# Kernel tuning notes

Measured on AMD Instinct MI355X. Metric: run time of the kernel, lower is better.

Reference implementation:

```python
import jax, jax.numpy as jnp
import numpy as np

B, T, D, K, CAND = 1024, 256, 128, 4, 500
NEG = float(-2**32 + 1)
EPS = 1e-3  # keras LayerNormalization default epsilon

def ln(x, g, b):
    mu = jnp.mean(x, axis=-1, keepdims=True)
    var = jnp.mean(jnp.square(x - mu), axis=-1, keepdims=True)
    return (x - mu) * jax.lax.rsqrt(var + EPS) * g + b

def setup_inputs() -> dict:
    key = jax.random.key(0)
    ks = jax.random.split(key, 12)
    s = 0.05
    inp = {
        'item_his_eb': jax.random.normal(ks[0], (B, T, D), jnp.float32),
        'mask': jax.random.randint(ks[1], (B, T), 0, 2, jnp.int32),
        'W1': jax.random.normal(ks[2], (D, D), jnp.float32) * s,
        'W2': jax.random.normal(ks[3], (D,), jnp.float32) * s,
        'W3': jax.random.normal(ks[4], (D, D), jnp.float32) * s,
        'W4': jax.random.normal(ks[5], (D,), jnp.float32) * s,
        'W_k1': jax.random.normal(ks[6], (K, D, D), jnp.float32) * s,
        'W_k2': jax.random.normal(ks[7], (K, D), jnp.float32) * s,
        'C': jax.random.normal(ks[8], (CAND, D), jnp.float32) * s,
        'pos_emb': jax.random.normal(ks[9], (1, T, D), jnp.float32) * s,
        'g1': jnp.ones((D,), jnp.float32), 'b1': jnp.zeros((D,), jnp.float32),
        'g2': jnp.ones((D,), jnp.float32), 'b2': jnp.zeros((D,), jnp.float32),
        'g3': jnp.ones((D,), jnp.float32), 'b3': jnp.zeros((D,), jnp.float32),
        'g4': jnp.ones((D,), jnp.float32), 'b4': jnp.zeros((D,), jnp.float32),
    }
    return inp

def reference(item_his_eb, mask, W1, W2, W3, W4, W_k1, W_k2, C, pos_emb,
              g1, b1, g2, b2, g3, b3, g4, b4):
    num_interest = W_k1.shape[0]
    m0 = (mask == 0)  # [B,T] padding positions
    x = item_his_eb + pos_emb  # [B,T,D]

    # Concept activation
    hidden = jnp.tanh(jnp.einsum('bte,ea->bta', x, W1))
    att = jnp.einsum('bte,e->bt', hidden, W2)
    a = jax.nn.softmax(jnp.where(m0, NEG, att), axis=-1)
    z_u = jnp.einsum('bte,bt->be', x, a)
    s_u = jnp.einsum('be,ce->bc', z_u, C)  # [B,CAND]
    s_u_k, idx = jax.lax.top_k(s_u, num_interest)  # sorted descending
    c_u = C[idx] * jax.nn.sigmoid(s_u_k)[..., None]  # [B,K,D]

    # Interest embedding generation
    h1 = jnp.einsum('bte,ea->bta', x, W3)
    h1 = jnp.einsum('bte,bke->btk', ln(h1, g1, b1), ln(c_u, g2, b2))
    h1 = jnp.where(m0[:, :, None], NEG, h1)
    P_kt = jnp.transpose(jax.nn.softmax(h1, axis=-1), (0, 2, 1))  # [B,K,T]
    h2 = jnp.tanh(jnp.einsum('bte,kea->bkta', x, W_k1))
    h2 = jnp.einsum('bkte,ke->bkt', h2, W_k2)
    h2 = jnp.where(m0[:, None, :], NEG, h2)
    P_tk = jax.nn.softmax(h2, axis=-1)  # softmax over t
    P = P_kt * P_tk
    interest_emb = ln(jnp.einsum('bte,bkt->bke', x, P), g3, b3)  # [B,K,D]

    # Interest aggregation
    P_u = jnp.transpose(P_kt, (0, 2, 1))  # [B,T,K]
    X_hat = jnp.einsum('btk,bke->bte', P_u, c_u)
    h3 = jnp.tanh(jnp.einsum('bte,ea->bta', X_hat, W3))
    h3 = jnp.einsum('bte,e->bt', h3, W4)
    h3 = jax.nn.softmax(jnp.where(m0, NEG, h3), axis=-1)
    c_apt = ln(jnp.einsum('bte,bt->be', X_hat, h3), g4, b4)
    e_u = jax.nn.softmax(jnp.einsum('be,bke->bk', c_apt, interest_emb) / 0.1, axis=-1)
    v_u = jnp.einsum('bke,bk->be', interest_emb, e_u)
    return v_u
```

## Files before the change

### kernel.cpp

```cpp
#include <hip/hip_runtime.h>
#include <hip/hip_bf16.h>
#include <string.h>

#define BB 1024
#define TT 256
#define DD 128
#define KK 4
#define CC 500
#define NEGF (-4294967296.0f)
#define EPSL 1e-3f

typedef __attribute__((ext_vector_type(8))) short bf16x8;
typedef __attribute__((ext_vector_type(4))) float f32x4;


__device__ __forceinline__ float fast_tanh(float x){
  float ax = fabsf(x);
  float e  = __expf(2.0f * ax);
  float t  = 1.0f - 2.0f * __builtin_amdgcn_rcpf(e + 1.0f);
  return copysignf(t, x);
}

__device__ __forceinline__ unsigned short bfbits(float f){
  __hip_bfloat16 h = __float2bfloat16(f);
  unsigned short u;
  memcpy(&u, &h, 2);
  return u;
}
__device__ __forceinline__ float bf2f(unsigned short u){
  return __uint_as_float(((unsigned)u) << 16);
}

__device__ __forceinline__ float wave_sum(float v){
  #pragma unroll
  for (int o = 32; o > 0; o >>= 1) v += __shfl_xor(v, o);
  return v;
}
__device__ __forceinline__ float wave_max(float v){
  #pragma unroll
  for (int o = 32; o > 0; o >>= 1) v = fmaxf(v, __shfl_xor(v, o));
  return v;
}


__global__ __launch_bounds__(256) void k_wpack(
    const float* __restrict__ W1, const float* __restrict__ W3,
    const float* __restrict__ Wk1,
    uint4* __restrict__ whi, uint4* __restrict__ wlo)
{
  int gid = blockIdx.x * 256 + threadIdx.x;
  int lane = gid & 63;
  int frag = gid >> 6;
  int n = frag & 7, kt = (frag >> 3) & 3, w = frag >> 5;
  const float* Wp = (w == 0) ? W1 : (w == 1) ? W3 : (Wk1 + (long)(w - 2) * DD * DD);
  int col = n * 16 + (lane & 15);
  int k0 = kt * 32 + (lane >> 4) * 8;
  unsigned int H[4], L[4];
  #pragma unroll
  for (int d = 0; d < 4; ++d){
    float v0 = Wp[(long)(k0 + 2 * d) * DD + col];
    float v1 = Wp[(long)(k0 + 2 * d + 1) * DD + col];
    unsigned short h0 = bfbits(v0); unsigned short l0 = bfbits(v0 - bf2f(h0));
    unsigned short h1 = bfbits(v1); unsigned short l1 = bfbits(v1 - bf2f(h1));
    H[d] = (unsigned)h0 | ((unsigned)h1 << 16);
    L[d] = (unsigned)l0 | ((unsigned)l1 << 16);
  }
  whi[gid] = make_uint4(H[0], H[1], H[2], H[3]);
  wlo[gid] = make_uint4(L[0], L[1], L[2], L[3]);
}


__global__ __launch_bounds__(256) void k_prep(
    const float* __restrict__ W3, const float* __restrict__ Cmat,
    float* __restrict__ W3T, float* __restrict__ CT)
{
  int gid = blockIdx.x * 256 + threadIdx.x;
  if (gid < DD * DD){
    int a = gid >> 7, e = gid & 127;
    W3T[gid] = W3[e * DD + a];
  } else {
    int j = gid - DD * DD;
    if (j < DD * CC){
      int e = j / CC, c = j - e * CC;
      CT[j] = Cmat[c * DD + e];
    }
  }
}


__global__ __launch_bounds__(512, 4) void k_big6m(
    const float* __restrict__ item, const float* __restrict__ pos,
    const uint4* __restrict__ whi, const uint4* __restrict__ wlo,
    const float* __restrict__ W2, const float* __restrict__ Wk2,
    float* __restrict__ att, float* __restrict__ h2log, float* __restrict__ lnstats)
{
  __shared__ uint4 smem4[4096];
  __shared__ float dscr[5][128][4];
  __shared__ float sscr[2][128][4];
  char* smem = (char*)smem4;
  const int tid = threadIdx.x, lane = tid & 63, wv = tid >> 6;
  const int ni = wv & 3, mi = wv >> 2;
  const long rbase = (long)blockIdx.x * 128;
  const int r15 = lane & 15, g = lane >> 4;
  const f32x4 ZV = {0.f, 0.f, 0.f, 0.f};

  #pragma unroll
  for (int it = 0; it < 4; ++it){
    int cid = tid + it * 512;
    int row = cid >> 4, c0 = (cid & 15) * 8;
    const float* src = item + (rbase + row) * DD + c0;
    const float* ps  = pos + (int)((rbase + row) & 255) * DD + c0;
    float4 f0 = *(const float4*)src;
    float4 f1 = *(const float4*)(src + 4);
    float4 p0 = *(const float4*)ps;
    float4 p1 = *(const float4*)(ps + 4);
    float v[8] = {f0.x + p0.x, f0.y + p0.y, f0.z + p0.z, f0.w + p0.w,
                  f1.x + p1.x, f1.y + p1.y, f1.z + p1.z, f1.w + p1.w};
    unsigned int H[4], L[4];
    #pragma unroll
    for (int d = 0; d < 4; ++d){
      unsigned short h0 = bfbits(v[2 * d]);     unsigned short l0 = bfbits(v[2 * d]     - bf2f(h0));
      unsigned short h1 = bfbits(v[2 * d + 1]); unsigned short l1 = bfbits(v[2 * d + 1] - bf2f(h1));
      H[d] = (unsigned)h0 | ((unsigned)h1 << 16);
      L[d] = (unsigned)l0 | ((unsigned)l1 << 16);
    }
    int byt = (c0 * 2) ^ ((row & 7) << 4);
    *(uint4*)(smem + row * 256 + byt)         = make_uint4(H[0], H[1], H[2], H[3]);
    *(uint4*)(smem + 32768 + row * 256 + byt) = make_uint4(L[0], L[1], L[2], L[3]);
  }
  __syncthreads();

  const int wrow = mi * 64;
  const int WL6[6] = {0, 2, 3, 4, 5, 1};

  #pragma unroll
  for (int wi = 0; wi < 6; ++wi){
    const int w = WL6[wi];
    f32x4 acc[4][2];
    #pragma unroll
    for (int m = 0; m < 4; ++m)
      #pragma unroll
      for (int n = 0; n < 2; ++n) acc[m][n] = ZV;

    #pragma unroll
    for (int kt = 0; kt < 4; ++kt){
      bf16x8 ah[4], al[4];
      #pragma unroll
      for (int m = 0; m < 4; ++m){
        int row = wrow + m * 16 + r15;
        int byt = (kt * 64 + g * 16) ^ ((row & 7) << 4);
        ah[m] = *(const bf16x8*)(smem + row * 256 + byt);
        al[m] = *(const bf16x8*)(smem + 32768 + row * 256 + byt);
      }
      const uint4* bhp = whi + (long)((w * 4 + kt) * 8 + ni * 2) * 64 + lane;
      const uint4* blp = wlo + (long)((w * 4 + kt) * 8 + ni * 2) * 64 + lane;
      #pragma unroll
      for (int n = 0; n < 2; ++n){
        uint4 bhu = bhp[n * 64], blu = blp[n * 64];
        bf16x8 bh = *(const bf16x8*)&bhu;
        bf16x8 bl = *(const bf16x8*)&blu;
        #pragma unroll
        for (int m = 0; m < 4; ++m){
          acc[m][n] = __builtin_amdgcn_mfma_f32_16x16x32_bf16(ah[m], bh, acc[m][n], 0, 0, 0);
          acc[m][n] = __builtin_amdgcn_mfma_f32_16x16x32_bf16(ah[m], bl, acc[m][n], 0, 0, 0);
          acc[m][n] = __builtin_amdgcn_mfma_f32_16x16x32_bf16(al[m], bh, acc[m][n], 0, 0, 0);
        }
      }
    }

    if (w != 1){
      const float* vp = (w == 0) ? W2 : (Wk2 + (w - 2) * DD);
      float pd[4][4] = {{0,0,0,0},{0,0,0,0},{0,0,0,0},{0,0,0,0}};
      #pragma unroll
      for (int n = 0; n < 2; ++n){
        float vv = vp[ni * 32 + n * 16 + r15];
        #pragma unroll
        for (int m = 0; m < 4; ++m)
          #pragma unroll
          for (int j = 0; j < 4; ++j)
            pd[m][j] = fmaf(fast_tanh(acc[m][n][j]), vv, pd[m][j]);
      }
      #pragma unroll
      for (int m = 0; m < 4; ++m)
        #pragma unroll
        for (int j = 0; j < 4; ++j){
          float v = pd[m][j];
          v += __shfl_xor(v, 1); v += __shfl_xor(v, 2);
          v += __shfl_xor(v, 4); v += __shfl_xor(v, 8);
          if (r15 == 0) dscr[wi][wrow + m * 16 + g * 4 + j][ni] = v;
        }
    } else {
      #pragma unroll
      for (int m = 0; m < 4; ++m)
        #pragma unroll
        for (int j = 0; j < 4; ++j){
          float s = 0.f, q = 0.f;
          #pragma unroll
          for (int n = 0; n < 2; ++n){
            float y = acc[m][n][j];
            s += y; q = fmaf(y, y, q);
          }
          s += __shfl_xor(s, 1); s += __shfl_xor(s, 2);
          s += __shfl_xor(s, 4); s += __shfl_xor(s, 8);
          q += __shfl_xor(q, 1); q += __shfl_xor(q, 2);
          q += __shfl_xor(q, 4); q += __shfl_xor(q, 8);
          if (r15 == 0){
            int row = wrow + m * 16 + g * 4 + j;
            sscr[0][row][ni] = s;
            sscr[1][row][ni] = q;
          }
        }
    }
  }
  __syncthreads();

  if (tid < 128){
    long rg = rbase + tid;
    long b = rg >> 8; int t = (int)(rg & 255);
    att[rg] = (dscr[0][tid][0] + dscr[0][tid][1]) + (dscr[0][tid][2] + dscr[0][tid][3]);
    #pragma unroll
    for (int wi = 1; wi < 5; ++wi)
      h2log[(b * KK + (wi - 1)) * TT + t] =
        (dscr[wi][tid][0] + dscr[wi][tid][1]) + (dscr[wi][tid][2] + dscr[wi][tid][3]);
    float s = (sscr[0][tid][0] + sscr[0][tid][1]) + (sscr[0][tid][2] + sscr[0][tid][3]);
    float q = (sscr[1][tid][0] + sscr[1][tid][1]) + (sscr[1][tid][2] + sscr[1][tid][3]);
    float mu = s * (1.f / DD);
    float var = q * (1.f / DD) - mu * mu;
    float rs = rsqrtf(var + EPSL);
    float2 st; st.x = mu; st.y = rs;
    *(float2*)&lnstats[rg * 2] = st;
  }
}


__global__ __launch_bounds__(256, 4) void k_fused(
    const float* __restrict__ item, const float* __restrict__ pos,
    const int* __restrict__ mask, const float* __restrict__ att,
    const float* __restrict__ h2log, const float* __restrict__ lnstats,
    const float* __restrict__ Cmat, const float* __restrict__ CT,
    const float* __restrict__ W3, const float* __restrict__ W3T,
    const float* __restrict__ g1, const float* __restrict__ b1,
    const float* __restrict__ g2, const float* __restrict__ b2,
    const float* __restrict__ g3, const float* __restrict__ b3,
    const float* __restrict__ g4, const float* __restrict__ b4,
    const float* __restrict__ W4, float* __restrict__ out)
{
  __shared__ float arena[4096];
  __shared__ float pkt_s[KK][TT];
  __shared__ float P_s[KK][TT];
  __shared__ float lnc_s[KK][DD];
  __shared__ float cu_s[KK][DD];
  __shared__ float vk_s[KK][DD];
  __shared__ float cw3s[KK][DD];
  __shared__ float ies_s[KK][DD];
  __shared__ float a_s[TT];
  __shared__ int   m0s[TT];
  __shared__ float g1s[DD], b1s[DD];
  __shared__ float cas[DD], w4s[DD];
  __shared__ float rbuf[32];
  __shared__ float sel_v[KK];
  __shared__ int   sel_i[KK];
  __shared__ float SkTk[2][KK];

  const int tid = threadIdx.x;
  const long b = blockIdx.x;
  const int lane = tid & 63, wv = tid >> 6;

  float attv = att[b * TT + tid];
  int   mk   = mask[b * TT + tid];
  if (tid < DD){ g1s[tid] = g1[tid]; b1s[tid] = b1[tid]; }
  m0s[tid] = (mk == 0);

  {
    float v = (mk == 0) ? NEGF : attv;
    float wm = wave_max(v);
    if (lane == 0) rbuf[wv] = wm;
    __syncthreads();
    float mx = fmaxf(fmaxf(rbuf[0], rbuf[1]), fmaxf(rbuf[2], rbuf[3]));
    float ex = __expf(v - mx);
    float ws = wave_sum(ex);
    if (lane == 0) rbuf[4 + wv] = ws;
    __syncthreads();
    float sm = rbuf[4] + rbuf[5] + rbuf[6] + rbuf[7];
    a_s[tid] = ex / sm;
  }
  __syncthreads();

  const float4* item4 = (const float4*)(item + (long)b * TT * DD);
  const float4* pos4  = (const float4*)pos;

  {
    int q = tid & 31, h = tid >> 5;
    float4 acc = {0.f, 0.f, 0.f, 0.f};
    for (int t = h; t < TT; t += 8){
      float4 xi = item4[t * 32 + q];
      float4 pp = pos4[t * 32 + q];
      float av = a_s[t];
      acc.x = fmaf(av, xi.x + pp.x, acc.x);
      acc.y = fmaf(av, xi.y + pp.y, acc.y);
      acc.z = fmaf(av, xi.z + pp.z, acc.z);
      acc.w = fmaf(av, xi.w + pp.w, acc.w);
    }
    *(float4*)&arena[h * 128 + q * 4] = acc;
    __syncthreads();
    if (tid < DD){
      float z = 0.f;
      #pragma unroll
      for (int h2 = 0; h2 < 8; ++h2) z += arena[h2 * 128 + tid];
      arena[1024 + tid] = z;
    }
    __syncthreads();
  }
  float* zs  = arena + 1024;
  float* s_s = arena + 1152;

  for (int c = tid; c < 512; c += 256){
    float s = -3.0e38f;
    if (c < CC){
      s = 0.f;
      for (int e = 0; e < DD; ++e) s = fmaf(zs[e], CT[e * CC + c], s);
    }
    s_s[c] = s;
  }
  __syncthreads();

  for (int k = 0; k < KK; ++k){
    float bv = -3.0e38f; int bi = 1 << 20;
    for (int c = tid; c < 512; c += 256){
      float sv = s_s[c];
      if (sv > bv || (sv == bv && c < bi)){ bv = sv; bi = c; }
    }
    #pragma unroll
    for (int o = 32; o > 0; o >>= 1){
      float ov = __shfl_xor(bv, o); int oi = __shfl_xor(bi, o);
      if (ov > bv || (ov == bv && oi < bi)){ bv = ov; bi = oi; }
    }
    if (lane == 0){ rbuf[wv] = bv; ((int*)rbuf)[8 + wv] = bi; }
    __syncthreads();
    if (tid == 0){
      float xv = rbuf[0]; int xi = ((int*)rbuf)[8];
      #pragma unroll
      for (int w2 = 1; w2 < 4; ++w2){
        float ov = rbuf[w2]; int oi = ((int*)rbuf)[8 + w2];
        if (ov > xv || (ov == xv && oi < xi)){ xv = ov; xi = oi; }
      }
      sel_v[k] = xv; sel_i[k] = xi; s_s[xi] = -3.0e38f;
    }
    __syncthreads();
  }

  {
    int k = wv, e0 = lane, e1 = lane + 64;
    float sig = 1.f / (1.f + __expf(-sel_v[k]));
    long ci = (long)sel_i[k] * DD;
    float c0 = Cmat[ci + e0] * sig, c1 = Cmat[ci + e1] * sig;
    cu_s[k][e0] = c0; cu_s[k][e1] = c1;
    float mean = wave_sum(c0 + c1) * (1.f / DD);
    float d0 = c0 - mean, d1 = c1 - mean;
    float var = wave_sum(d0 * d0 + d1 * d1) * (1.f / DD);
    float rs = rsqrtf(var + EPSL);
    float l0 = d0 * rs * g2[e0] + b2[e0];
    float l1 = d1 * rs * g2[e1] + b2[e1];
    lnc_s[k][e0] = l0; lnc_s[k][e1] = l1;
    float gl0 = g1s[e0] * l0, gl1 = g1s[e1] * l1;
    float S = wave_sum(gl0 + gl1);
    float T = wave_sum(b1s[e0] * l0 + b1s[e1] * l1);
    if (lane == 0){ SkTk[0][k] = S; SkTk[1][k] = T; }
    cw3s[k][e0] = gl0; cw3s[k][e1] = gl1;
    float v0 = 0.f, v1 = 0.f;
    for (int a = 0; a < DD; ++a){
      float gv = cw3s[k][a];
      v0 = fmaf(W3T[a * DD + e0], gv, v0);
      v1 = fmaf(W3T[a * DD + e1], gv, v1);
    }
    vk_s[k][e0] = v0; vk_s[k][e1] = v1;
  }
  __syncthreads();

  for (int step = 0; step < 16; ++step){
    int t = step * 16 + wv * 4 + (lane >> 4);
    int e0 = (lane & 15) * 8;
    const float* xr = item + ((long)b * TT + t) * DD + e0;
    const float* pr = pos + t * DD + e0;
    float4 xa = *(const float4*)xr, xb = *(const float4*)(xr + 4);
    float4 pa = *(const float4*)pr, pb = *(const float4*)(pr + 4);
    float x0 = xa.x + pa.x, x1 = xa.y + pa.y, x2 = xa.z + pa.z, x3 = xa.w + pa.w;
    float x4 = xb.x + pb.x, x5 = xb.y + pb.y, x6 = xb.z + pb.z, x7 = xb.w + pb.w;
    float2 st = *(const float2*)&lnstats[((long)b * TT + t) * 2];
    float h[KK];
    #pragma unroll
    for (int k = 0; k < KK; ++k){
      float4 v0 = *(const float4*)&vk_s[k][e0];
      float4 v1 = *(const float4*)&vk_s[k][e0 + 4];
      float pk = x0 * v0.x + x1 * v0.y + x2 * v0.z + x3 * v0.w
               + x4 * v1.x + x5 * v1.y + x6 * v1.z + x7 * v1.w;
      pk += __shfl_xor(pk, 1); pk += __shfl_xor(pk, 2);
      pk += __shfl_xor(pk, 4); pk += __shfl_xor(pk, 8);
      h[k] = st.y * (pk - st.x * SkTk[0][k]) + SkTk[1][k];
    }
    float p[KK];
    if (m0s[t]){
      p[0] = p[1] = p[2] = p[3] = 0.25f;
    } else {
      float mxh = fmaxf(fmaxf(h[0], h[1]), fmaxf(h[2], h[3]));
      float sme = 0.f;
      #pragma unroll
      for (int k = 0; k < KK; ++k){ p[k] = __expf(h[k] - mxh); sme += p[k]; }
      float inv = 1.f / sme;
      #pragma unroll
      for (int k = 0; k < KK; ++k) p[k] *= inv;
    }
    int kk = lane & 15;
    if (kk < KK) pkt_s[kk][t] = p[kk];
  }
  __syncthreads();

  {
    int k = wv;
    float4 vj = *(const float4*)&h2log[((long)b * KK + k) * TT + lane * 4];
    float v0 = m0s[lane * 4 + 0] ? NEGF : vj.x;
    float v1 = m0s[lane * 4 + 1] ? NEGF : vj.y;
    float v2 = m0s[lane * 4 + 2] ? NEGF : vj.z;
    float v3 = m0s[lane * 4 + 3] ? NEGF : vj.w;
    float mxv = wave_max(fmaxf(fmaxf(v0, v1), fmaxf(v2, v3)));
    float e0 = __expf(v0 - mxv), e1 = __expf(v1 - mxv);
    float e2 = __expf(v2 - mxv), e3 = __expf(v3 - mxv);
    float sm = wave_sum(e0 + e1 + e2 + e3);
    float inv = 1.f / sm;
    float4 pk4 = *(const float4*)&pkt_s[k][lane * 4];
    float4 r;
    r.x = pk4.x * e0 * inv; r.y = pk4.y * e1 * inv;
    r.z = pk4.z * e2 * inv; r.w = pk4.w * e3 * inv;
    *(float4*)&P_s[k][lane * 4] = r;
  }
  __syncthreads();

  {
    int q = tid & 31, h = tid >> 5;
    float4 ak[KK];
    #pragma unroll
    for (int k = 0; k < KK; ++k) ak[k] = {0.f, 0.f, 0.f, 0.f};
    for (int t = h; t < TT; t += 8){
      float4 xi = item4[t * 32 + q];
      float4 pp = pos4[t * 32 + q];
      float4 xv; xv.x = xi.x + pp.x; xv.y = xi.y + pp.y; xv.z = xi.z + pp.z; xv.w = xi.w + pp.w;
      #pragma unroll
      for (int k = 0; k < KK; ++k){
        float pv = P_s[k][t];
        ak[k].x = fmaf(pv, xv.x, ak[k].x); ak[k].y = fmaf(pv, xv.y, ak[k].y);
        ak[k].z = fmaf(pv, xv.z, ak[k].z); ak[k].w = fmaf(pv, xv.w, ak[k].w);
      }
    }
    #pragma unroll
    for (int k = 0; k < KK; ++k)
      *(float4*)&arena[h * 512 + k * 128 + q * 4] = ak[k];
    __syncthreads();
    int e = tid & 127, kh = tid >> 7;
    for (int k2 = kh; k2 < KK; k2 += 2){
      float s = 0.f;
      #pragma unroll
      for (int h2 = 0; h2 < 8; ++h2) s += arena[h2 * 512 + k2 * 128 + e];
      ies_s[k2][e] = s;
    }
  }
  __syncthreads();

  {
    int k = wv, e0 = lane, e1 = lane + 64;
    float v0 = ies_s[k][e0], v1 = ies_s[k][e1];
    float mean = wave_sum(v0 + v1) * (1.f / DD);
    float d0 = v0 - mean, d1 = v1 - mean;
    float var = wave_sum(d0 * d0 + d1 * d1) * (1.f / DD);
    float rs = rsqrtf(var + EPSL);
    ies_s[k][e0] = d0 * rs * g3[e0] + b3[e0];
    ies_s[k][e1] = d1 * rs * g3[e1] + b3[e1];
    float s0 = 0.f, s1 = 0.f;
    for (int e = 0; e < DD; ++e){
      float cv = cu_s[k][e];
      s0 = fmaf(cv, W3[e * DD + e0], s0);
      s1 = fmaf(cv, W3[e * DD + e1], s1);
    }
    cw3s[k][e0] = s0; cw3s[k][e1] = s1;
  }
  if (tid < DD) w4s[tid] = W4[tid];
  __syncthreads();

  float pk0 = pkt_s[0][tid], pk1 = pkt_s[1][tid], pk2 = pkt_s[2][tid], pk3 = pkt_s[3][tid];
  float sv = 0.f;
  for (int a = 0; a < DD; ++a){
    float hp = pk0 * cw3s[0][a] + pk1 * cw3s[1][a] + pk2 * cw3s[2][a] + pk3 * cw3s[3][a];
    sv = fmaf(fast_tanh(hp), w4s[a], sv);
  }
  float h3;
  {
    float v = m0s[tid] ? NEGF : sv;
    float wm = wave_max(v);
    if (lane == 0) rbuf[wv] = wm;
    __syncthreads();
    float mx = fmaxf(fmaxf(rbuf[0], rbuf[1]), fmaxf(rbuf[2], rbuf[3]));
    float ex = __expf(v - mx);
    float ws = wave_sum(ex);
    if (lane == 0) rbuf[4 + wv] = ws;
    __syncthreads();
    float sm = rbuf[4] + rbuf[5] + rbuf[6] + rbuf[7];
    h3 = ex / sm;
  }
  __syncthreads();
  {
    float w0 = wave_sum(pk0 * h3), w1 = wave_sum(pk1 * h3);
    float w2 = wave_sum(pk2 * h3), w3 = wave_sum(pk3 * h3);
    if (lane == 0){
      rbuf[8 + wv * 4 + 0] = w0; rbuf[8 + wv * 4 + 1] = w1;
      rbuf[8 + wv * 4 + 2] = w2; rbuf[8 + wv * 4 + 3] = w3;
    }
  }
  __syncthreads();
  float wk0 = rbuf[8] + rbuf[12] + rbuf[16] + rbuf[20];
  float wk1 = rbuf[9] + rbuf[13] + rbuf[17] + rbuf[21];
  float wk2 = rbuf[10] + rbuf[14] + rbuf[18] + rbuf[22];
  float wk3 = rbuf[11] + rbuf[15] + rbuf[19] + rbuf[23];
  {
    float cp = 0.f;
    if (tid < DD)
      cp = wk0 * cu_s[0][tid] + wk1 * cu_s[1][tid] + wk2 * cu_s[2][tid] + wk3 * cu_s[3][tid];
    float ws = wave_sum((tid < DD) ? cp : 0.f);
    if (lane == 0) rbuf[wv] = ws;
    __syncthreads();
    float mean = (rbuf[0] + rbuf[1] + rbuf[2] + rbuf[3]) * (1.f / DD);
    float d = (tid < DD) ? cp - mean : 0.f;
    float wq = wave_sum(d * d);
    if (lane == 0) rbuf[4 + wv] = wq;
    __syncthreads();
    float var = (rbuf[4] + rbuf[5] + rbuf[6] + rbuf[7]) * (1.f / DD);
    float rs = rsqrtf(var + EPSL);
    if (tid < DD) cas[tid] = d * rs * g4[tid] + b4[tid];
  }
  __syncthreads();
  {
    float c0 = (tid < DD) ? cas[tid] * ies_s[0][tid] : 0.f;
    float c1 = (tid < DD) ? cas[tid] * ies_s[1][tid] : 0.f;
    float c2 = (tid < DD) ? cas[tid] * ies_s[2][tid] : 0.f;
    float c3 = (tid < DD) ? cas[tid] * ies_s[3][tid] : 0.f;
    float w0 = wave_sum(c0), w1 = wave_sum(c1), w2 = wave_sum(c2), w3 = wave_sum(c3);
    if (lane == 0){
      rbuf[8 + wv * 4 + 0] = w0; rbuf[8 + wv * 4 + 1] = w1;
      rbuf[8 + wv * 4 + 2] = w2; rbuf[8 + wv * 4 + 3] = w3;
    }
    __syncthreads();
    float l0 = (rbuf[8] + rbuf[12] + rbuf[16] + rbuf[20]) * 10.f;
    float l1 = (rbuf[9] + rbuf[13] + rbuf[17] + rbuf[21]) * 10.f;
    float l2 = (rbuf[10] + rbuf[14] + rbuf[18] + rbuf[22]) * 10.f;
    float l3 = (rbuf[11] + rbuf[15] + rbuf[19] + rbuf[23]) * 10.f;
    float mx2 = fmaxf(fmaxf(l0, l1), fmaxf(l2, l3));
    float e0 = __expf(l0 - mx2), e1 = __expf(l1 - mx2);
    float e2 = __expf(l2 - mx2), e3 = __expf(l3 - mx2);
    float inv = 1.f / (e0 + e1 + e2 + e3);
    if (tid < DD){
      float r = (ies_s[0][tid] * e0 + ies_s[1][tid] * e1 +
                 ies_s[2][tid] * e2 + ies_s[3][tid] * e3) * inv;
      out[b * DD + tid] = r;
    }
  }
}


extern "C" void kernel_launch(void* const* d_in, const int* in_sizes, int n_in,
                              void* d_out, int out_size, void* d_ws, size_t ws_size,
                              hipStream_t stream)
{
  const float* item = (const float*)d_in[0];
  const int*   mask = (const int*)d_in[1];
  const float* W1   = (const float*)d_in[2];
  const float* W2   = (const float*)d_in[3];
  const float* W3   = (const float*)d_in[4];
  const float* W4   = (const float*)d_in[5];
  const float* Wk1  = (const float*)d_in[6];
  const float* Wk2  = (const float*)d_in[7];
  const float* Cm   = (const float*)d_in[8];
  const float* pos  = (const float*)d_in[9];
  const float* g1   = (const float*)d_in[10]; const float* b1 = (const float*)d_in[11];
  const float* g2   = (const float*)d_in[12]; const float* b2 = (const float*)d_in[13];
  const float* g3   = (const float*)d_in[14]; const float* b3 = (const float*)d_in[15];
  const float* g4   = (const float*)d_in[16]; const float* b4 = (const float*)d_in[17];
  float* out = (float*)d_out;

  char* p = (char*)d_ws;
  float* att     = (float*)(p);
  float* h2log   = (float*)(p + 1048576);
  float* lnstats = (float*)(p + 5242880);
  float* W3T     = (float*)(p + 7340032);
  float* CT      = (float*)(p + 7405568);
  uint4* whi = (uint4*)d_out;
  uint4* wlo = whi + 12288;
  (void)in_sizes; (void)n_in; (void)out_size; (void)ws_size;

  k_wpack <<<dim3(48),  dim3(256), 0, stream>>>(W1, W3, Wk1, whi, wlo);
  k_prep  <<<dim3(314), dim3(256), 0, stream>>>(W3, Cm, W3T, CT);
  k_big6m <<<dim3((BB * TT) / 128), dim3(512), 0, stream>>>(item, pos, whi, wlo, W2, Wk2,
                                                            att, h2log, lnstats);
  k_fused <<<dim3(BB), dim3(256), 0, stream>>>(item, pos, mask, att, h2log, lnstats,
                                               Cm, CT, W3, W3T,
                                               g1, b1, g2, b2, g3, b3, g4, b4, W4, out);
}
```

Baseline: 299.1 us.

## Halve big6m row tile to 64, retile waves, merge prep kernels

The two small weight-prep kernels are merged into one launch to cut launch overhead. The main projection kernel now processes 64 rows per block instead of 128, with 8 waves split 4 (rows) x 2 (columns). Each wave computes a 16x64 output tile instead of 64x32. This halves LDS and accumulator registers so launch bounds can request 8 blocks per CU for higher occupancy, at the cost of less A-fragment reuse and doubled B-weight global loads per row.

```diff
diff --git a/kernel.cpp b/kernel.cpp
--- a/kernel.cpp
+++ b/kernel.cpp
@@ -7,6 +7,7 @@
 #define DD 128
 #define KK 4
 #define CC 500
+#define BR 64
 #define NEGF (-4294967296.0f)
 #define EPSL 1e-3f
 
@@ -43,69 +44,66 @@
 }
 
 
-__global__ __launch_bounds__(256) void k_wpack(
+__global__ __launch_bounds__(256) void k_preppack(
     const float* __restrict__ W1, const float* __restrict__ W3,
-    const float* __restrict__ Wk1,
-    uint4* __restrict__ whi, uint4* __restrict__ wlo)
-{
-  int gid = blockIdx.x * 256 + threadIdx.x;
-  int lane = gid & 63;
-  int frag = gid >> 6;
-  int n = frag & 7, kt = (frag >> 3) & 3, w = frag >> 5;
-  const float* Wp = (w == 0) ? W1 : (w == 1) ? W3 : (Wk1 + (long)(w - 2) * DD * DD);
-  int col = n * 16 + (lane & 15);
-  int k0 = kt * 32 + (lane >> 4) * 8;
-  unsigned int H[4], L[4];
-  #pragma unroll
-  for (int d = 0; d < 4; ++d){
-    float v0 = Wp[(long)(k0 + 2 * d) * DD + col];
-    float v1 = Wp[(long)(k0 + 2 * d + 1) * DD + col];
-    unsigned short h0 = bfbits(v0); unsigned short l0 = bfbits(v0 - bf2f(h0));
-    unsigned short h1 = bfbits(v1); unsigned short l1 = bfbits(v1 - bf2f(h1));
-    H[d] = (unsigned)h0 | ((unsigned)h1 << 16);
-    L[d] = (unsigned)l0 | ((unsigned)l1 << 16);
-  }
-  whi[gid] = make_uint4(H[0], H[1], H[2], H[3]);
-  wlo[gid] = make_uint4(L[0], L[1], L[2], L[3]);
-}
-
-
-__global__ __launch_bounds__(256) void k_prep(
-    const float* __restrict__ W3, const float* __restrict__ Cmat,
+    const float* __restrict__ Wk1, const float* __restrict__ Cmat,
+    uint4* __restrict__ whi, uint4* __restrict__ wlo,
     float* __restrict__ W3T, float* __restrict__ CT)
 {
   int gid = blockIdx.x * 256 + threadIdx.x;
-  if (gid < DD * DD){
-    int a = gid >> 7, e = gid & 127;
-    W3T[gid] = W3[e * DD + a];
+  if (gid < 12288){
+    int lane = gid & 63;
+    int frag = gid >> 6;
+    int n = frag & 7, kt = (frag >> 3) & 3, w = frag >> 5;
+    const float* Wp = (w == 0) ? W1 : (w == 1) ? W3 : (Wk1 + (long)(w - 2) * DD * DD);
+    int col = n * 16 + (lane & 15);
+    int k0 = kt * 32 + (lane >> 4) * 8;
+    unsigned int H[4], L[4];
+    #pragma unroll
+    for (int d = 0; d < 4; ++d){
+      float v0 = Wp[(long)(k0 + 2 * d) * DD + col];
+      float v1 = Wp[(long)(k0 + 2 * d + 1) * DD + col];
+      unsigned short h0 = bfbits(v0); unsigned short l0 = bfbits(v0 - bf2f(h0));
+      unsigned short h1 = bfbits(v1); unsigned short l1 = bfbits(v1 - bf2f(h1));
+      H[d] = (unsigned)h0 | ((unsigned)h1 << 16);
+      L[d] = (unsigned)l0 | ((unsigned)l1 << 16);
+    }
+    whi[gid] = make_uint4(H[0], H[1], H[2], H[3]);
+    wlo[gid] = make_uint4(L[0], L[1], L[2], L[3]);
   } else {
-    int j = gid - DD * DD;
-    if (j < DD * CC){
-      int e = j / CC, c = j - e * CC;
-      CT[j] = Cmat[c * DD + e];
-    }
-  }
-}
-
-
-__global__ __launch_bounds__(512, 4) void k_big6m(
+    int j = gid - 12288;
+    if (j < DD * DD){
+      int a = j >> 7, e = j & 127;
+      W3T[j] = W3[e * DD + a];
+    } else {
+      j -= DD * DD;
+      if (j < DD * CC){
+        int e = j / CC, c = j - e * CC;
+        CT[j] = Cmat[c * DD + e];
+      }
+    }
+  }
+}
+
+
+__global__ __launch_bounds__(512, 8) void k_big6m(
     const float* __restrict__ item, const float* __restrict__ pos,
     const uint4* __restrict__ whi, const uint4* __restrict__ wlo,
     const float* __restrict__ W2, const float* __restrict__ Wk2,
     float* __restrict__ att, float* __restrict__ h2log, float* __restrict__ lnstats)
 {
-  __shared__ uint4 smem4[4096];
-  __shared__ float dscr[5][128][4];
-  __shared__ float sscr[2][128][4];
+  __shared__ uint4 smem4[2048];
+  __shared__ float dscr[5][BR][2];
+  __shared__ float sscr[2][BR][2];
   char* smem = (char*)smem4;
   const int tid = threadIdx.x, lane = tid & 63, wv = tid >> 6;
-  const int ni = wv & 3, mi = wv >> 2;
-  const long rbase = (long)blockIdx.x * 128;
+  const int ni = wv & 1, mi = wv >> 1;
+  const long rbase = (long)blockIdx.x * BR;
   const int r15 = lane & 15, g = lane >> 4;
   const f32x4 ZV = {0.f, 0.f, 0.f, 0.f};
 
   #pragma unroll
-  for (int it = 0; it < 4; ++it){
+  for (int it = 0; it < 2; ++it){
     int cid = tid + it * 512;
     int row = cid >> 4, c0 = (cid & 15) * 8;
     const float* src = item + (rbase + row) * DD + c0;
@@ -126,104 +124,88 @@
     }
     int byt = (c0 * 2) ^ ((row & 7) << 4);
     *(uint4*)(smem + row * 256 + byt)         = make_uint4(H[0], H[1], H[2], H[3]);
-    *(uint4*)(smem + 32768 + row * 256 + byt) = make_uint4(L[0], L[1], L[2], L[3]);
-  }
-  __syncthreads();
-
-  const int wrow = mi * 64;
+    *(uint4*)(smem + 16384 + row * 256 + byt) = make_uint4(L[0], L[1], L[2], L[3]);
+  }
+  __syncthreads();
+
+  const int wrow = mi * 16;
   const int WL6[6] = {0, 2, 3, 4, 5, 1};
 
   #pragma unroll
   for (int wi = 0; wi < 6; ++wi){
     const int w = WL6[wi];
-    f32x4 acc[4][2];
-    #pragma unroll
-    for (int m = 0; m < 4; ++m)
-      #pragma unroll
-      for (int n = 0; n < 2; ++n) acc[m][n] = ZV;
+    f32x4 acc[4];
+    #pragma unroll
+    for (int n = 0; n < 4; ++n) acc[n] = ZV;
 
     #pragma unroll
     for (int kt = 0; kt < 4; ++kt){
-      bf16x8 ah[4], al[4];
-      #pragma unroll
-      for (int m = 0; m < 4; ++m){
-        int row = wrow + m * 16 + r15;
-        int byt = (kt * 64 + g * 16) ^ ((row & 7) << 4);
-        ah[m] = *(const bf16x8*)(smem + row * 256 + byt);
-        al[m] = *(const bf16x8*)(smem + 32768 + row * 256 + byt);
-      }
-      const uint4* bhp = whi + (long)((w * 4 + kt) * 8 + ni * 2) * 64 + lane;
-      const uint4* blp = wlo + (long)((w * 4 + kt) * 8 + ni * 2) * 64 + lane;
-      #pragma unroll
-      for (int n = 0; n < 2; ++n){
+      int row = wrow + r15;
+      int byt = (kt * 64 + g * 16) ^ ((row & 7) << 4);
+      bf16x8 ah = *(const bf16x8*)(smem + row * 256 + byt);
+      bf16x8 al = *(const bf16x8*)(smem + 16384 + row * 256 + byt);
+      const uint4* bhp = whi + (long)((w * 4 + kt) * 8 + ni * 4) * 64 + lane;
+      const uint4* blp = wlo + (long)((w * 4 + kt) * 8 + ni * 4) * 64 + lane;
+      #pragma unroll
+      for (int n = 0; n < 4; ++n){
         uint4 bhu = bhp[n * 64], blu = blp[n * 64];
         bf16x8 bh = *(const bf16x8*)&bhu;
         bf16x8 bl = *(const bf16x8*)&blu;
-        #pragma unroll
-        for (int m = 0; m < 4; ++m){
-          acc[m][n] = __builtin_amdgcn_mfma_f32_16x16x32_bf16(ah[m], bh, acc[m][n], 0, 0, 0);
-          acc[m][n] = __builtin_amdgcn_mfma_f32_16x16x32_bf16(ah[m], bl, acc[m][n], 0, 0, 0);
-          acc[m][n] = __builtin_amdgcn_mfma_f32_16x16x32_bf16(al[m], bh, acc[m][n], 0, 0, 0);
-        }
+        acc[n] = __builtin_amdgcn_mfma_f32_16x16x32_bf16(ah, bh, acc[n], 0, 0, 0);
+        acc[n] = __builtin_amdgcn_mfma_f32_16x16x32_bf16(ah, bl, acc[n], 0, 0, 0);
+        acc[n] = __builtin_amdgcn_mfma_f32_16x16x32_bf16(al, bh, acc[n], 0, 0, 0);
       }
     }
 
     if (w != 1){
       const float* vp = (w == 0) ? W2 : (Wk2 + (w - 2) * DD);
-      float pd[4][4] = {{0,0,0,0},{0,0,0,0},{0,0,0,0},{0,0,0,0}};
-      #pragma unroll
-      for (int n = 0; n < 2; ++n){
-        float vv = vp[ni * 32 + n * 16 + r15];
+      float pd[4] = {0.f, 0.f, 0.f, 0.f};
+      #pragma unroll
+      for (int n = 0; n < 4; ++n){
+        float vv = vp[ni * 64 + n * 16 + r15];
         #pragma unroll
-        for (int m = 0; m < 4; ++m)
-          #pragma unroll
-          for (int j = 0; j < 4; ++j)
-            pd[m][j] = fmaf(fast_tanh(acc[m][n][j]), vv, pd[m][j]);
-      }
-      #pragma unroll
-      for (int m = 0; m < 4; ++m)
+        for (int j = 0; j < 4; ++j)
+          pd[j] = fmaf(fast_tanh(acc[n][j]), vv, pd[j]);
+      }
+      #pragma unroll
+      for (int j = 0; j < 4; ++j){
+        float v = pd[j];
+        v += __shfl_xor(v, 1); v += __shfl_xor(v, 2);
+        v += __shfl_xor(v, 4); v += __shfl_xor(v, 8);
+        if (r15 == 0) dscr[wi][wrow + g * 4 + j][ni] = v;
+      }
+    } else {
+      #pragma unroll
+      for (int j = 0; j < 4; ++j){
+        float s = 0.f, q = 0.f;
         #pragma unroll
-        for (int j = 0; j < 4; ++j){
-          float v = pd[m][j];
-          v += __shfl_xor(v, 1); v += __shfl_xor(v, 2);
-          v += __shfl_xor(v, 4); v += __shfl_xor(v, 8);
-          if (r15 == 0) dscr[wi][wrow + m * 16 + g * 4 + j][ni] = v;
+        for (int n = 0; n < 4; ++n){
+          float y = acc[n][j];
+          s += y; q = fmaf(y, y, q);
         }
-    } else {
-      #pragma unroll
-      for (int m = 0; m < 4; ++m)
-        #pragma unroll
-        for (int j = 0; j < 4; ++j){
-          float s = 0.f, q = 0.f;
-          #pragma unroll
-          for (int n = 0; n < 2; ++n){
-            float y = acc[m][n][j];
-            s += y; q = fmaf(y, y, q);
-          }
-          s += __shfl_xor(s, 1); s += __shfl_xor(s, 2);
-          s += __shfl_xor(s, 4); s += __shfl_xor(s, 8);
-          q += __shfl_xor(q, 1); q += __shfl_xor(q, 2);
-          q += __shfl_xor(q, 4); q += __shfl_xor(q, 8);
-          if (r15 == 0){
-            int row = wrow + m * 16 + g * 4 + j;
-            sscr[0][row][ni] = s;
-            sscr[1][row][ni] = q;
-          }
+        s += __shfl_xor(s, 1); s += __shfl_xor(s, 2);
+        s += __shfl_xor(s, 4); s += __shfl_xor(s, 8);
+        q += __shfl_xor(q, 1); q += __shfl_xor(q, 2);
+        q += __shfl_xor(q, 4); q += __shfl_xor(q, 8);
+        if (r15 == 0){
+          int row = wrow + g * 4 + j;
+          sscr[0][row][ni] = s;
+          sscr[1][row][ni] = q;
         }
-    }
-  }
-  __syncthreads();
-
-  if (tid < 128){
+      }
+    }
+  }
+  __syncthreads();
+
+  if (tid < BR){
     long rg = rbase + tid;
     long b = rg >> 8; int t = (int)(rg & 255);
-    att[rg] = (dscr[0][tid][0] + dscr[0][tid][1]) + (dscr[0][tid][2] + dscr[0][tid][3]);
+    att[rg] = dscr[0][tid][0] + dscr[0][tid][1];
     #pragma unroll
     for (int wi = 1; wi < 5; ++wi)
-      h2log[(b * KK + (wi - 1)) * TT + t] =
-        (dscr[wi][tid][0] + dscr[wi][tid][1]) + (dscr[wi][tid][2] + dscr[wi][tid][3]);
-    float s = (sscr[0][tid][0] + sscr[0][tid][1]) + (sscr[0][tid][2] + sscr[0][tid][3]);
-    float q = (sscr[1][tid][0] + sscr[1][tid][1]) + (sscr[1][tid][2] + sscr[1][tid][3]);
+      h2log[(b * KK + (wi - 1)) * TT + t] = dscr[wi][tid][0] + dscr[wi][tid][1];
+    float s = sscr[0][tid][0] + sscr[0][tid][1];
+    float q = sscr[1][tid][0] + sscr[1][tid][1];
     float mu = s * (1.f / DD);
     float var = q * (1.f / DD) - mu * mu;
     float rs = rsqrtf(var + EPSL);
@@ -594,11 +576,10 @@
   uint4* wlo = whi + 12288;
   (void)in_sizes; (void)n_in; (void)out_size; (void)ws_size;
 
-  k_wpack <<<dim3(48),  dim3(256), 0, stream>>>(W1, W3, Wk1, whi, wlo);
-  k_prep  <<<dim3(314), dim3(256), 0, stream>>>(W3, Cm, W3T, CT);
-  k_big6m <<<dim3((BB * TT) / 128), dim3(512), 0, stream>>>(item, pos, whi, wlo, W2, Wk2,
-                                                            att, h2log, lnstats);
-  k_fused <<<dim3(BB), dim3(256), 0, stream>>>(item, pos, mask, att, h2log, lnstats,
-                                               Cm, CT, W3, W3T,
-                                               g1, b1, g2, b2, g3, b3, g4, b4, W4, out);
-}
+  k_preppack <<<dim3(362), dim3(256), 0, stream>>>(W1, W3, Wk1, Cm, whi, wlo, W3T, CT);
+  k_big6m    <<<dim3((BB * TT) / BR), dim3(512), 0, stream>>>(item, pos, whi, wlo, W2, Wk2,
+                                                              att, h2log, lnstats);
+  k_fused    <<<dim3(BB), dim3(256), 0, stream>>>(item, pos, mask, att, h2log, lnstats,
+                                                  Cm, CT, W3, W3T,
+                                                  g1, b1, g2, b2, g3, b3, g4, b4, W4, out);
+}
```

After: 347.2 us. +16.1%, slower.
